# Performance work log

Measured on AMD Instinct MI355X. Metric: run time of the kernel, lower is better.

Reference implementation:

```python
import jax, jax.numpy as jnp
import numpy as np

N, D, H = 16384, 128, 512
C = 1.0          # curvature c_in
EPS_GIN = 0.0    # GIN epsilon
MIN_NORM = 1e-7


def _arcosh(z):
    z = jnp.clip(z, 1.0 + MIN_NORM, None)
    return jnp.log(z + jnp.sqrt(z * z - 1.0))


def exp_map_zero(u, c):
    # hyperboloid exp at origin; tangent 'time' coord u[...,0] is ignored
    sqrtK = 1.0 / jnp.sqrt(c)
    x = u[..., 1:]
    n = jnp.clip(jnp.linalg.norm(x, axis=-1, keepdims=True), MIN_NORM, None)
    theta = n / sqrtK
    return jnp.concatenate(
        [sqrtK * jnp.cosh(theta), sqrtK * jnp.sinh(theta) * x / n], axis=-1)


def log_map_zero(p, c):
    # hyperboloid log at origin; result has zero 'time' coord
    sqrtK = 1.0 / jnp.sqrt(c)
    y = p[..., 1:]
    n = jnp.clip(jnp.linalg.norm(y, axis=-1, keepdims=True), MIN_NORM, None)
    theta = _arcosh(p[..., :1] / sqrtK)
    return jnp.concatenate(
        [jnp.zeros_like(theta), sqrtK * theta * y / n], axis=-1)


def setup_inputs() -> dict:
    key = jax.random.key(0)
    k1, k2, k3, k4 = jax.random.split(key, 4)
    x = jax.random.normal(k1, (N, D), dtype=jnp.float32)
    adj = jax.random.uniform(k2, (N, N), dtype=jnp.float32) / N  # row-normalized-ish
    W1 = jax.random.normal(k3, (D, H), dtype=jnp.float32) * (1.0 / np.sqrt(D))
    b1 = jnp.zeros((H,), dtype=jnp.float32)
    W2 = jax.random.normal(k4, (H, D), dtype=jnp.float32) * (1.0 / np.sqrt(H))
    b2 = jnp.zeros((D,), dtype=jnp.float32)
    return {"x": x, "adj": adj, "W1": W1, "b1": b1, "W2": W2, "b2": b2}


def reference(x, adj, W1, b1, W2, b2):
    # 1) lift features onto hyperboloid
    h = exp_map_zero(x, C)                       # [N, D]
    # 2) LorentzAgg (no attention): aggregate in tangent space at origin
    agg = exp_map_zero(adj @ log_map_zero(h, C), C)   # [N, D]
    # 3) GIN combine in tangent space: log(out) + (1+eps)*log(x_r), then exp
    out = exp_map_zero(log_map_zero(agg, C) + (1.0 + EPS_GIN) * log_map_zero(h, C), C)
    # 4) GIN MLP
    t = jax.nn.relu(out @ W1 + b1) @ W2 + b2     # [N, D]
    return t
```

## Files before the change

kernel.cpp:

```cpp
#include <hip/hip_runtime.h>

#define GN 16384
#define GD 128
#define GH 512
#define GK 16384

#define SPLITS 2
#define SKK (GK / SPLITS)
#define BM 64
#define BK 64

typedef __attribute__((ext_vector_type(8))) short s8v;
typedef __attribute__((ext_vector_type(4))) float f4v;
typedef __attribute__((ext_vector_type(4))) int   i4v;

#define AS1 __attribute__((address_space(1)))
#define AS3 __attribute__((address_space(3)))

static __device__ inline unsigned short f2bf(float f) {
  union { float f; unsigned u; } a; a.f = f;
  unsigned r = a.u + 0x7fffu + ((a.u >> 16) & 1u);
  return (unsigned short)(r >> 16);
}

static __device__ inline unsigned cvtpk(float lo, float hi) {
  unsigned r;
  asm("v_cvt_pk_bf16_f32 %0, %1, %2" : "=v"(r) : "v"(lo), "v"(hi));
  return r;
}

static __device__ inline float waveAllSum(float v) {
  #pragma unroll
  for (int off = 32; off; off >>= 1) v += __shfl_xor(v, off);
  return v;
}

__global__ void k_logmap(const float* __restrict__ x, float* __restrict__ Lf) {
  int row  = (blockIdx.x << 2) + (threadIdx.x >> 6);
  int lane = threadIdx.x & 63;
  size_t base = ((size_t)row << 7) + (lane << 1);
  float2 v = *(const float2*)(x + base);
  float a0 = (lane == 0) ? 0.f : v.x;
  float a1 = v.y;
  float n = fmaxf(sqrtf(waveAllSum(a0*a0 + a1*a1)), 1e-7f);
  float sh = sinhf(n), ch = coshf(n);
  float y0 = sh * a0 / n, y1 = sh * a1 / n;
  float ny = fmaxf(sqrtf(waveAllSum(y0*y0 + y1*y1)), 1e-7f);
  float z  = fmaxf(ch, 1.f + 1e-7f);
  float th = logf(z + sqrtf(z*z - 1.f));
  float l0 = th * y0 / ny;
  float l1 = th * y1 / ny;
  if (lane == 0) l0 = 0.f;
  *(float2*)(Lf + base) = make_float2(l0, l1);
}

__global__ void k_tconv(const float* __restrict__ src, unsigned short* __restrict__ dst,
                        int NR, int NC) {
  __shared__ float tile[64][65];
  const int r0 = blockIdx.x << 6;
  const int c0 = blockIdx.y << 6;
  const int t  = threadIdx.x;
  const int r  = t >> 2;
  const int cg = (t & 3) << 4;
  const float* s = src + (size_t)(r0 + r) * NC + c0 + cg;
  #pragma unroll
  for (int j = 0; j < 4; ++j) {
    float4 f = ((const float4*)s)[j];
    tile[r][cg + 4*j + 0] = f.x;
    tile[r][cg + 4*j + 1] = f.y;
    tile[r][cg + 4*j + 2] = f.z;
    tile[r][cg + 4*j + 3] = f.w;
  }
  __syncthreads();
  s8v o0, o1;
  #pragma unroll
  for (int j = 0; j < 8; ++j) o0[j] = (short)f2bf(tile[cg + j][r]);
  #pragma unroll
  for (int j = 0; j < 8; ++j) o1[j] = (short)f2bf(tile[cg + 8 + j][r]);
  unsigned short* d = dst + (size_t)(c0 + r) * NR + r0 + cg;
  *(s8v*)d = o0;
  *((s8v*)d + 1) = o1;
}

#define ASZ (BM * BK * 4)
#define BSZ (128 * BK * 2)
#define BUFSZ (ASZ + BSZ)
__global__ __launch_bounds__(512) void k_gemm(const float* __restrict__ adj,
    const unsigned short* __restrict__ Lt, float* __restrict__ Mpart) {
  __shared__ __align__(16) char lds[2 * BUFSZ];
  const int tid  = threadIdx.x;
  const int lane = tid & 63, wid = tid >> 6;
  const int wr = wid >> 2, wn = wid & 3;
  const int l15 = lane & 15, lhi = (lane >> 4) << 3;
  const int bid = blockIdx.x;
  const int split = bid & 1, rowblk = bid >> 1;
  const size_t blockRow = (size_t)rowblk * BM;
  const size_t k0 = (size_t)split * SKK;

  f4v acc[2][2];
  #pragma unroll
  for (int m = 0; m < 2; ++m)
    #pragma unroll
    for (int n = 0; n < 2; ++n) acc[m][n] = (f4v){0.f, 0.f, 0.f, 0.f};

  const int rA = tid >> 4, gA = tid & 15;
  const float* aSrc = adj + (blockRow + rA) * (size_t)GK + k0
                      + (size_t)((gA ^ (rA & 7)) << 2);
  const int rB = tid >> 3, gB = tid & 7;
  const unsigned short* bSrc = Lt + (size_t)rB * GK + k0
                               + (size_t)((gB ^ (rB & 7)) << 3);

  const int NIT = SKK / BK;

#define STAGE(c, itv)                                                          \
  {                                                                            \
    const float*          ap = aSrc + (size_t)(itv) * BK;                      \
    const unsigned short* bp = bSrc + (size_t)(itv) * BK;                      \
    char* ab = lds + (c) * BUFSZ;                                              \
    char* bb = lds + (c) * BUFSZ + ASZ;                                        \
    _Pragma("unroll")                                                          \
    for (int j = 0; j < 2; ++j)                                                \
      __builtin_amdgcn_global_load_lds(                                        \
        (const AS1 void*)(ap + (size_t)j * 32 * GK),                           \
        (AS3 void*)(ab + ((tid + j * 512) << 4)), 16, 0, 0);                   \
    _Pragma("unroll")                                                          \
    for (int j = 0; j < 2; ++j)                                                \
      __builtin_amdgcn_global_load_lds(                                        \
        (const AS1 void*)(bp + (size_t)j * 64 * GK),                           \
        (AS3 void*)(bb + ((tid + j * 512) << 4)), 16, 0, 0);                   \
  }

  int cur = 0;
  STAGE(0, 0);
  __syncthreads();

  for (int it = 0; it < NIT; ++it) {
    if (it + 1 < NIT) STAGE(cur ^ 1, it + 1);

    const char* ab = lds + cur * BUFSZ;
    const char* bb = lds + cur * BUFSZ + ASZ;
    #pragma unroll
    for (int ks = 0; ks < 2; ++ks) {
      s8v bfr[2];
      #pragma unroll
      for (int n = 0; n < 2; ++n) {
        int rowb = 32*wn + 16*n + l15;
        int gb   = (4*ks + (lhi >> 3)) ^ (rowb & 7);
        bfr[n] = *(const s8v*)(bb + rowb * 128 + (gb << 4));
      }
      #pragma unroll
      for (int m = 0; m < 2; ++m) {
        int rowa = 32*wr + 16*m + l15;
        int ga0  = 8*ks + (lhi >> 2);
        int sw   = rowa & 7;
        f4v x0 = *(const f4v*)(ab + rowa * 256 + ((ga0       ^ sw) << 4));
        f4v x1 = *(const f4v*)(ab + rowa * 256 + (((ga0 + 1) ^ sw) << 4));
        union { unsigned u[4]; s8v v; } ua;
        ua.u[0] = cvtpk(x0[0], x0[1]);
        ua.u[1] = cvtpk(x0[2], x0[3]);
        ua.u[2] = cvtpk(x1[0], x1[1]);
        ua.u[3] = cvtpk(x1[2], x1[3]);
        acc[m][0] = __builtin_amdgcn_mfma_f32_16x16x32_bf16(ua.v, bfr[0], acc[m][0], 0, 0, 0);
        acc[m][1] = __builtin_amdgcn_mfma_f32_16x16x32_bf16(ua.v, bfr[1], acc[m][1], 0, 0, 0);
      }
    }
    __syncthreads();
    cur ^= 1;
  }
#undef STAGE

  float* mp = Mpart + (size_t)split * GN * GD;
  #pragma unroll
  for (int m = 0; m < 2; ++m)
    #pragma unroll
    for (int n = 0; n < 2; ++n) {
      size_t r0 = blockRow + 32*wr + 16*m + ((lane >> 4) << 2);
      int    c0 = 32*wn + 16*n + l15;
      #pragma unroll
      for (int j = 0; j < 4; ++j)
        mp[(r0 + j) * GD + c0] = acc[m][n][j];
    }
}

__global__ void k_maps(const float* __restrict__ Mp, const float* __restrict__ Lf,
                       unsigned short* __restrict__ outB) {
  int row  = (blockIdx.x << 2) + (threadIdx.x >> 6);
  int lane = threadIdx.x & 63;
  size_t base = ((size_t)row << 7) + (lane << 1);
  const size_t PS = (size_t)GN * GD;
  float2 m0 = *(const float2*)(Mp + base);
  float2 m1 = *(const float2*)(Mp + PS + base);
  float mvx = m0.x + m1.x;
  float mvy = m0.y + m1.y;
  float2 lv = *(const float2*)(Lf + base);
  float v0 = (lane == 0) ? 0.f : mvx;
  float v1 = mvy;
  float nv = fmaxf(sqrtf(waveAllSum(v0*v0 + v1*v1)), 1e-7f);
  float ch = coshf(nv), sh = sinhf(nv);
  float g0 = sh * v0 / nv, g1 = sh * v1 / nv;
  float ny = fmaxf(sqrtf(waveAllSum(g0*g0 + g1*g1)), 1e-7f);
  float z  = fmaxf(ch, 1.f + 1e-7f);
  float th = logf(z + sqrtf(z*z - 1.f));
  float la0 = th * g0 / ny, la1 = th * g1 / ny;
  float s0 = la0 + lv.x, s1 = la1 + lv.y;
  if (lane == 0) s0 = 0.f;
  float ns  = fmaxf(sqrtf(waveAllSum(s0*s0 + s1*s1)), 1e-7f);
  float ch2 = coshf(ns), sh2 = sinhf(ns);
  float o0 = sh2 * s0 / ns, o1 = sh2 * s1 / ns;
  if (lane == 0) o0 = ch2;
  unsigned pack = (unsigned)f2bf(o0) | ((unsigned)f2bf(o1) << 16);
  *(unsigned*)(outB + base) = pack;
}

#define PAD1 136
#define PADH 520
__global__ __launch_bounds__(256, 2) void k_mlp(const unsigned short* __restrict__ outB,
    const unsigned short* __restrict__ W1t, const float* __restrict__ b1,
    const unsigned short* __restrict__ W2t, const float* __restrict__ b2,
    float* __restrict__ Tout) {
  __shared__ __align__(16) short sA[32 * PAD1];
  __shared__ __align__(16) short sH[32 * PADH];
  const int tid  = threadIdx.x;
  const int lane = tid & 63, wc = tid >> 6;
  const int row0 = blockIdx.x << 5;

  {
    const int r = tid >> 3, cg = (tid & 7) << 4;
    const unsigned short* src = outB + (size_t)(row0 + r) * GD + cg;
    i4v v0 = ((const i4v*)src)[0];
    i4v v1 = ((const i4v*)src)[1];
    *(i4v*)&sA[r * PAD1 + cg]     = v0;
    *(i4v*)&sA[r * PAD1 + cg + 8] = v1;
  }
  __syncthreads();

  f4v acc1[2][8];
  #pragma unroll
  for (int mi = 0; mi < 2; ++mi)
    #pragma unroll
    for (int ni = 0; ni < 8; ++ni) acc1[mi][ni] = (f4v){0.f,0.f,0.f,0.f};

  const int afr = (lane & 15) * PAD1 + ((lane >> 4) << 3);
  #pragma unroll
  for (int kk = 0; kk < 4; ++kk) {
    s8v a0 = *(const s8v*)&sA[afr + kk*32];
    s8v a1 = *(const s8v*)&sA[afr + 16*PAD1 + kk*32];
    #pragma unroll
    for (int ni = 0; ni < 8; ++ni) {
      const unsigned short* bp = W1t + (size_t)(128*wc + 16*ni + (lane & 15)) * GD
                                 + ((lane >> 4) << 3) + kk*32;
      s8v b = *(const s8v*)bp;
      acc1[0][ni] = __builtin_amdgcn_mfma_f32_16x16x32_bf16(a0, b, acc1[0][ni], 0, 0, 0);
      acc1[1][ni] = __builtin_amdgcn_mfma_f32_16x16x32_bf16(a1, b, acc1[1][ni], 0, 0, 0);
    }
  }
  #pragma unroll
  for (int ni = 0; ni < 8; ++ni) {
    int col = 128*wc + 16*ni + (lane & 15);
    float bb = b1[col];
    #pragma unroll
    for (int mi = 0; mi < 2; ++mi) {
      #pragma unroll
      for (int j = 0; j < 4; ++j) {
        int row = 16*mi + ((lane >> 4) << 2) + j;
        float v = fmaxf(acc1[mi][ni][j] + bb, 0.f);
        sH[row * PADH + col] = (short)f2bf(v);
      }
    }
  }
  __syncthreads();

  f4v acc2[2][2];
  #pragma unroll
  for (int mi = 0; mi < 2; ++mi)
    #pragma unroll
    for (int ni = 0; ni < 2; ++ni) acc2[mi][ni] = (f4v){0.f,0.f,0.f,0.f};

  const int hfr = (lane & 15) * PADH + ((lane >> 4) << 3);
  #pragma unroll
  for (int kk = 0; kk < 16; ++kk) {
    s8v a0 = *(const s8v*)&sH[hfr + kk*32];
    s8v a1 = *(const s8v*)&sH[hfr + 16*PADH + kk*32];
    #pragma unroll
    for (int ni = 0; ni < 2; ++ni) {
      const unsigned short* bp = W2t + (size_t)(32*wc + 16*ni + (lane & 15)) * GH
                                 + ((lane >> 4) << 3) + kk*32;
      s8v b = *(const s8v*)bp;
      acc2[0][ni] = __builtin_amdgcn_mfma_f32_16x16x32_bf16(a0, b, acc2[0][ni], 0, 0, 0);
      acc2[1][ni] = __builtin_amdgcn_mfma_f32_16x16x32_bf16(a1, b, acc2[1][ni], 0, 0, 0);
    }
  }
  #pragma unroll
  for (int mi = 0; mi < 2; ++mi)
    #pragma unroll
    for (int ni = 0; ni < 2; ++ni) {
      int c0 = 32*wc + 16*ni + (lane & 15);
      float bb = b2[c0];
      size_t r0 = row0 + 16*mi + ((lane >> 4) << 2);
      #pragma unroll
      for (int j = 0; j < 4; ++j)
        Tout[(r0 + j) * GD + c0] = acc2[mi][ni][j] + bb;
    }
}

extern "C" void kernel_launch(void* const* d_in, const int* in_sizes, int n_in,
                              void* d_out, int out_size, void* d_ws, size_t ws_size,
                              hipStream_t stream) {
  const float* x   = (const float*)d_in[0];
  const float* adj = (const float*)d_in[1];
  const float* W1  = (const float*)d_in[2];
  const float* b1  = (const float*)d_in[3];
  const float* W2  = (const float*)d_in[4];
  const float* b2  = (const float*)d_in[5];
  float* Tout = (float*)d_out;

  char* ws = (char*)d_ws;
  float*          Lf    = (float*)ws;
  unsigned short* Lt    = (unsigned short*)(ws + (8u  << 20));
  float*          Mpart = (float*)(ws + (12u << 20));
  unsigned short* outB  = (unsigned short*)(ws + (28u << 20));
  unsigned short* W1t   = (unsigned short*)(ws + (32u << 20));
  unsigned short* W2t   = (unsigned short*)(ws + (32u << 20) + (128u << 10));

  k_logmap <<<GN / 4, 256, 0, stream>>>(x, Lf);
  k_tconv  <<<dim3(GK / 64, GD / 64), 256, 0, stream>>>(Lf, Lt, GN, GD);
  k_tconv  <<<dim3(GD / 64, GH / 64), 256, 0, stream>>>(W1, W1t, GD, GH);
  k_tconv  <<<dim3(GH / 64, GD / 64), 256, 0, stream>>>(W2, W2t, GH, GD);
  k_gemm   <<<(GN / BM) * SPLITS, 512, 0, stream>>>(adj, Lt, Mpart);
  k_maps   <<<GN / 4, 256, 0, stream>>>(Mpart, Lf, outB);
  k_mlp    <<<GN / 32, 256, 0, stream>>>(outB, W1t, b1, W2t, b2, Tout);
}
```

Measured before the change: 256.8 us.

## Halve GEMM row tile and load B fragments directly from global into registers

The adjacency GEMM now uses 32-row tiles with 256-thread blocks, and each wave covers 32 output columns. The B operand (transposed log-map features) is no longer staged through LDS. Each thread loads its MFMA fragments straight from global memory into registers, double-buffered across iterations. This shrinks LDS use and doubles the grid, aiming for better occupancy and less LDS traffic on a kernel bound by streaming adj. In exchange, B is re-read from global/L2 by every block with uncoalesced 16-byte row-strided loads.

```diff
diff --git a/kernel.cpp b/kernel.cpp
--- a/kernel.cpp
+++ b/kernel.cpp
@@ -7,7 +7,7 @@
 
 #define SPLITS 2
 #define SKK (GK / SPLITS)
-#define BM 64
+#define BM 32
 #define BK 64
 
 typedef __attribute__((ext_vector_type(8))) short s8v;
@@ -83,15 +83,12 @@
 }
 
 #define ASZ (BM * BK * 4)
-#define BSZ (128 * BK * 2)
-#define BUFSZ (ASZ + BSZ)
-__global__ __launch_bounds__(512) void k_gemm(const float* __restrict__ adj,
+__global__ __launch_bounds__(256, 2) void k_gemm(const float* __restrict__ adj,
     const unsigned short* __restrict__ Lt, float* __restrict__ Mpart) {
-  __shared__ __align__(16) char lds[2 * BUFSZ];
+  __shared__ __align__(16) char lds[2 * ASZ];
   const int tid  = threadIdx.x;
-  const int lane = tid & 63, wid = tid >> 6;
-  const int wr = wid >> 2, wn = wid & 3;
-  const int l15 = lane & 15, lhi = (lane >> 4) << 3;
+  const int lane = tid & 63, wn = tid >> 6;
+  const int l15 = lane & 15, hi = lane >> 4;
   const int bid = blockIdx.x;
   const int split = bid & 1, rowblk = bid >> 1;
   const size_t blockRow = (size_t)rowblk * BM;
@@ -106,52 +103,55 @@
   const int rA = tid >> 4, gA = tid & 15;
   const float* aSrc = adj + (blockRow + rA) * (size_t)GK + k0
                       + (size_t)((gA ^ (rA & 7)) << 2);
-  const int rB = tid >> 3, gB = tid & 7;
-  const unsigned short* bSrc = Lt + (size_t)rB * GK + k0
-                               + (size_t)((gB ^ (rB & 7)) << 3);
+
+  const unsigned short* bB[2][2];
+  #pragma unroll
+  for (int ks = 0; ks < 2; ++ks)
+    #pragma unroll
+    for (int n = 0; n < 2; ++n)
+      bB[ks][n] = Lt + (size_t)(32*wn + 16*n + l15) * GK + k0 + 32*ks + 8*hi;
 
   const int NIT = SKK / BK;
 
 #define STAGE(c, itv)                                                          \
   {                                                                            \
-    const float*          ap = aSrc + (size_t)(itv) * BK;                      \
-    const unsigned short* bp = bSrc + (size_t)(itv) * BK;                      \
-    char* ab = lds + (c) * BUFSZ;                                              \
-    char* bb = lds + (c) * BUFSZ + ASZ;                                        \
+    const float* ap = aSrc + (size_t)(itv) * BK;                               \
+    char* ab = lds + (c) * ASZ;                                                \
     _Pragma("unroll")                                                          \
     for (int j = 0; j < 2; ++j)                                                \
       __builtin_amdgcn_global_load_lds(                                        \
-        (const AS1 void*)(ap + (size_t)j * 32 * GK),                           \
-        (AS3 void*)(ab + ((tid + j * 512) << 4)), 16, 0, 0);                   \
+        (const AS1 void*)(ap + (size_t)j * 16 * GK),                           \
+        (AS3 void*)(ab + ((tid + j * 256) << 4)), 16, 0, 0);                   \
+  }
+
+#define BLOAD(dst, itv)                                                        \
+  {                                                                            \
     _Pragma("unroll")                                                          \
-    for (int j = 0; j < 2; ++j)                                                \
-      __builtin_amdgcn_global_load_lds(                                        \
-        (const AS1 void*)(bp + (size_t)j * 64 * GK),                           \
-        (AS3 void*)(bb + ((tid + j * 512) << 4)), 16, 0, 0);                   \
-  }
-
+    for (int ks = 0; ks < 2; ++ks)                                             \
+      _Pragma("unroll")                                                        \
+      for (int n = 0; n < 2; ++n)                                              \
+        dst[ks][n] = *(const s8v*)(bB[ks][n] + (size_t)(itv) * BK);            \
+  }
+
+  s8v bcur[2][2], bnext[2][2];
   int cur = 0;
   STAGE(0, 0);
+  BLOAD(bcur, 0);
   __syncthreads();
 
   for (int it = 0; it < NIT; ++it) {
-    if (it + 1 < NIT) STAGE(cur ^ 1, it + 1);
-
-    const char* ab = lds + cur * BUFSZ;
-    const char* bb = lds + cur * BUFSZ + ASZ;
+    if (it + 1 < NIT) {
+      STAGE(cur ^ 1, it + 1);
+      BLOAD(bnext, it + 1);
+    }
+
+    const char* ab = lds + cur * ASZ;
     #pragma unroll
     for (int ks = 0; ks < 2; ++ks) {
-      s8v bfr[2];
-      #pragma unroll
-      for (int n = 0; n < 2; ++n) {
-        int rowb = 32*wn + 16*n + l15;
-        int gb   = (4*ks + (lhi >> 3)) ^ (rowb & 7);
-        bfr[n] = *(const s8v*)(bb + rowb * 128 + (gb << 4));
-      }
       #pragma unroll
       for (int m = 0; m < 2; ++m) {
-        int rowa = 32*wr + 16*m + l15;
-        int ga0  = 8*ks + (lhi >> 2);
+        int rowa = 16*m + l15;
+        int ga0  = 8*ks + 2*hi;
         int sw   = rowa & 7;
         f4v x0 = *(const f4v*)(ab + rowa * 256 + ((ga0       ^ sw) << 4));
         f4v x1 = *(const f4v*)(ab + rowa * 256 + (((ga0 + 1) ^ sw) << 4));
@@ -160,21 +160,26 @@
         ua.u[1] = cvtpk(x0[2], x0[3]);
         ua.u[2] = cvtpk(x1[0], x1[1]);
         ua.u[3] = cvtpk(x1[2], x1[3]);
-        acc[m][0] = __builtin_amdgcn_mfma_f32_16x16x32_bf16(ua.v, bfr[0], acc[m][0], 0, 0, 0);
-        acc[m][1] = __builtin_amdgcn_mfma_f32_16x16x32_bf16(ua.v, bfr[1], acc[m][1], 0, 0, 0);
+        acc[m][0] = __builtin_amdgcn_mfma_f32_16x16x32_bf16(ua.v, bcur[ks][0], acc[m][0], 0, 0, 0);
+        acc[m][1] = __builtin_amdgcn_mfma_f32_16x16x32_bf16(ua.v, bcur[ks][1], acc[m][1], 0, 0, 0);
       }
     }
     __syncthreads();
+    #pragma unroll
+    for (int ks = 0; ks < 2; ++ks)
+      #pragma unroll
+      for (int n = 0; n < 2; ++n) bcur[ks][n] = bnext[ks][n];
     cur ^= 1;
   }
 #undef STAGE
+#undef BLOAD
 
   float* mp = Mpart + (size_t)split * GN * GD;
   #pragma unroll
   for (int m = 0; m < 2; ++m)
     #pragma unroll
     for (int n = 0; n < 2; ++n) {
-      size_t r0 = blockRow + 32*wr + 16*m + ((lane >> 4) << 2);
+      size_t r0 = blockRow + 16*m + (hi << 2);
       int    c0 = 32*wn + 16*n + l15;
       #pragma unroll
       for (int j = 0; j < 4; ++j)
@@ -326,7 +331,7 @@
   k_tconv  <<<dim3(GK / 64, GD / 64), 256, 0, stream>>>(Lf, Lt, GN, GD);
   k_tconv  <<<dim3(GD / 64, GH / 64), 256, 0, stream>>>(W1, W1t, GD, GH);
   k_tconv  <<<dim3(GH / 64, GD / 64), 256, 0, stream>>>(W2, W2t, GH, GD);
-  k_gemm   <<<(GN / BM) * SPLITS, 512, 0, stream>>>(adj, Lt, Mpart);
+  k_gemm   <<<(GN / BM) * SPLITS, 256, 0, stream>>>(adj, Lt, Mpart);
   k_maps   <<<GN / 4, 256, 0, stream>>>(Mpart, Lf, outB);
   k_mlp    <<<GN / 32, 256, 0, stream>>>(outB, W1t, b1, W2t, b2, Tout);
 }
```

Measured after the change: 384.0 us. +49.6%, slower.

## Retile adjacency GEMM to 128-row blocks, BK=32, and four K-splits

Applied to the files above, without the earlier changes.

Changes the main adj@L GEMM tiling from 64-row blocks with BK=64 and 2 K-splits to 128-row blocks with BK=32 and 4 K-splits. Warps are rearranged 4x2, each computing 32x64 outputs with more MFMAs per fragment load, and the LDS swizzle is redone for the narrower B tile. The aim is to halve how often the bf16 L operand is reloaded per adj row and keep the block count the same. The cost is double the partial-sum output traffic, so k_maps now reduces four partials, and the workspace offsets move to fit the larger partial buffer.

```diff
diff --git a/kernel.cpp b/kernel.cpp
--- a/kernel.cpp
+++ b/kernel.cpp
@@ -5,10 +5,10 @@
 #define GH 512
 #define GK 16384
 
-#define SPLITS 2
+#define SPLITS 4
 #define SKK (GK / SPLITS)
-#define BM 64
-#define BK 64
+#define BM 128
+#define BK 32
 
 typedef __attribute__((ext_vector_type(8))) short s8v;
 typedef __attribute__((ext_vector_type(4))) float f4v;
@@ -90,25 +90,26 @@
   __shared__ __align__(16) char lds[2 * BUFSZ];
   const int tid  = threadIdx.x;
   const int lane = tid & 63, wid = tid >> 6;
-  const int wr = wid >> 2, wn = wid & 3;
-  const int l15 = lane & 15, lhi = (lane >> 4) << 3;
+  const int wm = wid >> 1, wn = wid & 1;
+  const int l15 = lane & 15, hi = lane >> 4;
   const int bid = blockIdx.x;
-  const int split = bid & 1, rowblk = bid >> 1;
+  const int split = bid & 3, rowblk = bid >> 2;
   const size_t blockRow = (size_t)rowblk * BM;
   const size_t k0 = (size_t)split * SKK;
 
-  f4v acc[2][2];
+  f4v acc[2][4];
   #pragma unroll
   for (int m = 0; m < 2; ++m)
     #pragma unroll
-    for (int n = 0; n < 2; ++n) acc[m][n] = (f4v){0.f, 0.f, 0.f, 0.f};
-
-  const int rA = tid >> 4, gA = tid & 15;
+    for (int n = 0; n < 4; ++n) acc[m][n] = (f4v){0.f, 0.f, 0.f, 0.f};
+
+  const int rA = tid >> 3, gA = tid & 7;
   const float* aSrc = adj + (blockRow + rA) * (size_t)GK + k0
                       + (size_t)((gA ^ (rA & 7)) << 2);
-  const int rB = tid >> 3, gB = tid & 7;
+  const int rB = tid >> 2, gB = tid & 3;
+  const int swB0 = (rB ^ (rB >> 2)) & 3;
   const unsigned short* bSrc = Lt + (size_t)rB * GK + k0
-                               + (size_t)((gB ^ (rB & 7)) << 3);
+                               + (size_t)((gB ^ swB0) << 3);
 
   const int NIT = SKK / BK;
 
@@ -121,13 +122,11 @@
     _Pragma("unroll")                                                          \
     for (int j = 0; j < 2; ++j)                                                \
       __builtin_amdgcn_global_load_lds(                                        \
-        (const AS1 void*)(ap + (size_t)j * 32 * GK),                           \
+        (const AS1 void*)(ap + (size_t)j * 64 * GK),                           \
         (AS3 void*)(ab + ((tid + j * 512) << 4)), 16, 0, 0);                   \
-    _Pragma("unroll")                                                          \
-    for (int j = 0; j < 2; ++j)                                                \
-      __builtin_amdgcn_global_load_lds(                                        \
-        (const AS1 void*)(bp + (size_t)j * 64 * GK),                           \
-        (AS3 void*)(bb + ((tid + j * 512) << 4)), 16, 0, 0);                   \
+    __builtin_amdgcn_global_load_lds(                                          \
+        (const AS1 void*)bp,                                                   \
+        (AS3 void*)(bb + (tid << 4)), 16, 0, 0);                               \
   }
 
   int cur = 0;
@@ -139,30 +138,28 @@
 
     const char* ab = lds + cur * BUFSZ;
     const char* bb = lds + cur * BUFSZ + ASZ;
-    #pragma unroll
-    for (int ks = 0; ks < 2; ++ks) {
-      s8v bfr[2];
+    s8v bfr[4];
+    #pragma unroll
+    for (int n = 0; n < 4; ++n) {
+      int rowb = 64*wn + 16*n + l15;
+      int gb   = hi ^ ((rowb ^ (rowb >> 2)) & 3);
+      bfr[n] = *(const s8v*)(bb + rowb * 64 + (gb << 4));
+    }
+    #pragma unroll
+    for (int m = 0; m < 2; ++m) {
+      int rowa = 32*wm + 16*m + l15;
+      int ga0  = 2*hi;
+      int sw   = rowa & 7;
+      f4v x0 = *(const f4v*)(ab + rowa * 128 + ((ga0       ^ sw) << 4));
+      f4v x1 = *(const f4v*)(ab + rowa * 128 + (((ga0 + 1) ^ sw) << 4));
+      union { unsigned u[4]; s8v v; } ua;
+      ua.u[0] = cvtpk(x0[0], x0[1]);
+      ua.u[1] = cvtpk(x0[2], x0[3]);
+      ua.u[2] = cvtpk(x1[0], x1[1]);
+      ua.u[3] = cvtpk(x1[2], x1[3]);
       #pragma unroll
-      for (int n = 0; n < 2; ++n) {
-        int rowb = 32*wn + 16*n + l15;
-        int gb   = (4*ks + (lhi >> 3)) ^ (rowb & 7);
-        bfr[n] = *(const s8v*)(bb + rowb * 128 + (gb << 4));
-      }
-      #pragma unroll
-      for (int m = 0; m < 2; ++m) {
-        int rowa = 32*wr + 16*m + l15;
-        int ga0  = 8*ks + (lhi >> 2);
-        int sw   = rowa & 7;
-        f4v x0 = *(const f4v*)(ab + rowa * 256 + ((ga0       ^ sw) << 4));
-        f4v x1 = *(const f4v*)(ab + rowa * 256 + (((ga0 + 1) ^ sw) << 4));
-        union { unsigned u[4]; s8v v; } ua;
-        ua.u[0] = cvtpk(x0[0], x0[1]);
-        ua.u[1] = cvtpk(x0[2], x0[3]);
-        ua.u[2] = cvtpk(x1[0], x1[1]);
-        ua.u[3] = cvtpk(x1[2], x1[3]);
-        acc[m][0] = __builtin_amdgcn_mfma_f32_16x16x32_bf16(ua.v, bfr[0], acc[m][0], 0, 0, 0);
-        acc[m][1] = __builtin_amdgcn_mfma_f32_16x16x32_bf16(ua.v, bfr[1], acc[m][1], 0, 0, 0);
-      }
+      for (int n = 0; n < 4; ++n)
+        acc[m][n] = __builtin_amdgcn_mfma_f32_16x16x32_bf16(ua.v, bfr[n], acc[m][n], 0, 0, 0);
     }
     __syncthreads();
     cur ^= 1;
@@ -173,9 +170,9 @@
   #pragma unroll
   for (int m = 0; m < 2; ++m)
     #pragma unroll
-    for (int n = 0; n < 2; ++n) {
-      size_t r0 = blockRow + 32*wr + 16*m + ((lane >> 4) << 2);
-      int    c0 = 32*wn + 16*n + l15;
+    for (int n = 0; n < 4; ++n) {
+      size_t r0 = blockRow + 32*wm + 16*m + (hi << 2);
+      int    c0 = 64*wn + 16*n + l15;
       #pragma unroll
       for (int j = 0; j < 4; ++j)
         mp[(r0 + j) * GD + c0] = acc[m][n][j];
@@ -190,8 +187,10 @@
   const size_t PS = (size_t)GN * GD;
   float2 m0 = *(const float2*)(Mp + base);
   float2 m1 = *(const float2*)(Mp + PS + base);
-  float mvx = m0.x + m1.x;
-  float mvy = m0.y + m1.y;
+  float2 m2 = *(const float2*)(Mp + 2*PS + base);
+  float2 m3 = *(const float2*)(Mp + 3*PS + base);
+  float mvx = (m0.x + m1.x) + (m2.x + m3.x);
+  float mvy = (m0.y + m1.y) + (m2.y + m3.y);
   float2 lv = *(const float2*)(Lf + base);
   float v0 = (lane == 0) ? 0.f : mvx;
   float v1 = mvy;
@@ -318,9 +317,9 @@
   float*          Lf    = (float*)ws;
   unsigned short* Lt    = (unsigned short*)(ws + (8u  << 20));
   float*          Mpart = (float*)(ws + (12u << 20));
-  unsigned short* outB  = (unsigned short*)(ws + (28u << 20));
-  unsigned short* W1t   = (unsigned short*)(ws + (32u << 20));
-  unsigned short* W2t   = (unsigned short*)(ws + (32u << 20) + (128u << 10));
+  unsigned short* outB  = (unsigned short*)(ws + (44u << 20));
+  unsigned short* W1t   = (unsigned short*)(ws + (48u << 20));
+  unsigned short* W2t   = (unsigned short*)(ws + (48u << 20) + (128u << 10));
 
   k_logmap <<<GN / 4, 256, 0, stream>>>(x, Lf);
   k_tconv  <<<dim3(GK / 64, GD / 64), 256, 0, stream>>>(Lf, Lt, GN, GD);
```

Measured after the change: 267.3 us. 1.04x slower.
